# Performance work log

Measured on AMD Instinct MI355X. Metric: run time of the kernel, lower is better.

The kernel has to match this reference:

```python
import jax, jax.numpy as jnp
import numpy as np

B, M, D = 16384, 32, 16
LAYERS = [64, 64, 64]


def setup_inputs() -> dict:
    key = jax.random.key(0)
    ks = jax.random.split(key, 4)
    inp = {"embeddings": jax.random.normal(ks[0], (B, M, D), dtype=jnp.float32)}
    hk_1 = M
    for i, hk in enumerate(LAYERS):
        # glorot-ish scale for W_i of shape (m, Hk_1, Hk)
        scale = (2.0 / (M * hk_1 + hk)) ** 0.5
        inp[f"W{i}"] = jax.random.normal(ks[i + 1], (M, hk_1, hk), dtype=jnp.float32) * scale
        hk_1 = hk
    return inp


def reference(embeddings, W0, W1, W2):
    # embeddings == x0: (B, m, D); W_i: (m, Hk_1, Hk)
    x0 = embeddings
    xk = x0  # x^{k-1}, starts as x0 with Hk_1 = m
    outs = []
    for W in (W0, W1, W2):
        # Fused form of: (x0[:,:,None,:] * xk[:,None,:,:])[..., None] * W -> sum over m, Hk_1
        # then permute to (B, Hk, D) and apply activation.
        xk = jax.nn.relu(jnp.einsum("bmd,bhd,mhk->bkd", x0, xk, W))  # (B, Hk, D)
        outs.append(jnp.sum(xk, axis=2))  # (B, Hk)
    return jnp.concatenate(outs, axis=1)  # (B, sum(layers_dim))
```

## Files before the change

### kernel.cpp

```cpp
#include <hip/hip_runtime.h>


typedef _Float16 half8 __attribute__((ext_vector_type(8)));
typedef _Float16 half2v __attribute__((ext_vector_type(2)));
typedef float f32x4 __attribute__((ext_vector_type(4)));

#define OUT_STRIDE 192
#define X0R 32
#define X0B 512
#define XKR 72
#define XKB 1152

__global__ void prep_w_all(const float* __restrict__ W0,
                           const float* __restrict__ W1,
                           const float* __restrict__ W2,
                           _Float16* __restrict__ dst) {
  int e = blockIdx.x * 256 + threadIdx.x;
  const float* W;
  int logH, nkbLog, le;
  if (e < 65536)       { W = W0; logH = 5; nkbLog = 5; le = e; }
  else if (e < 196608) { W = W1; logH = 6; nkbLog = 6; le = e - 65536; }
  else                 { W = W2; logH = 6; nkbLog = 6; le = e - 196608; }
  int j    = le & 7;
  int lane = (le >> 3) & 63;
  int rr   = lane & 15, qq = lane >> 4;
  int rest = le >> 9;
  int kb   = rest & ((1 << nkbLog) - 1);
  int t    = rest >> nkbLog;
  int k    = kb * 32 + qq * 8 + j;
  int H    = 1 << logH;
  int m    = k >> logH, h = k & (H - 1);
  int n    = t * 16 + rr;
  dst[e] = (_Float16)W[(m * H + h) * 64 + n];
}

template<int NHI, bool LAST>
__device__ __forceinline__ void run_layer(
    const _Float16* __restrict__ Wp, const half8 (&av)[4][NHI],
    const _Float16* x0s, _Float16* xkw, float* __restrict__ out,
    long gb0, int loff, int lane, int r, int q)
{
  const int NKB = 32 * NHI;
  f32x4 acc[4][4];
#pragma unroll
  for (int b = 0; b < 4; ++b)
#pragma unroll
    for (int t = 0; t < 4; ++t) acc[b][t] = (f32x4){0.f, 0.f, 0.f, 0.f};

  const _Float16* Wl = Wp + lane * 8;

#pragma unroll 2
  for (int m = 0; m < 32; ++m) {
    half2v xs2[4];
#pragma unroll
    for (int b = 0; b < 4; ++b) {
      _Float16 x = x0s[b * X0B + r * X0R + m];
      xs2[b] = (half2v){x, x};
    }
#pragma unroll
    for (int hi = 0; hi < NHI; ++hi) {
      const int kb = m * NHI + hi;
      half8 Bf[4];
#pragma unroll
      for (int t = 0; t < 4; ++t)
        Bf[t] = *(const half8*)(Wl + (size_t)(t * NKB + kb) * 512);
#pragma unroll
      for (int b = 0; b < 4; ++b) {
        half8 af;
        half2v* ap = (half2v*)&af;
        const half2v* vp = (const half2v*)&av[b][hi];
#pragma unroll
        for (int j2 = 0; j2 < 4; ++j2) ap[j2] = vp[j2] * xs2[b];
#pragma unroll
        for (int t = 0; t < 4; ++t)
          acc[b][t] = __builtin_amdgcn_mfma_f32_16x16x32_f16(
              af, Bf[t], acc[b][t], 0, 0, 0);
      }
    }
  }

#pragma unroll
  for (int b = 0; b < 4; ++b) {
#pragma unroll
    for (int t = 0; t < 4; ++t) {
      float s = 0.f;
#pragma unroll
      for (int rr = 0; rr < 4; ++rr) {
        float v = acc[b][t][rr];
        v = v > 0.f ? v : 0.f;
        s += v;
        if (!LAST)
          xkw[b * XKB + (q * 4 + rr) * XKR + t * 16 + r] = (_Float16)v;
      }
      s += __shfl_xor(s, 16);
      s += __shfl_xor(s, 32);
      if (q == 0)
        out[(gb0 + b) * OUT_STRIDE + loff + t * 16 + r] = s;
    }
  }
}

__global__ __launch_bounds__(256, 3) void cin_main(
    const float* __restrict__ emb, const _Float16* __restrict__ Wall,
    float* __restrict__ out)
{
  __shared__ __align__(16) _Float16 lds[16 * X0B + 16 * XKB];
  const int lane = threadIdx.x & 63;
  const int wv = threadIdx.x >> 6;
  const int r = lane & 15, q = lane >> 4;
  const long gb0 = (long)blockIdx.x * 16 + wv * 4;

  _Float16* x0w = &lds[wv * 4 * X0B];
  _Float16* xkw = &lds[16 * X0B + wv * 4 * XKB];

#pragma unroll
  for (int bb = 0; bb < 4; ++bb) {
    const float* src = emb + (gb0 + bb) * 512;
    _Float16* dstb = x0w + bb * X0B;
#pragma unroll
    for (int i = 0; i < 2; ++i) {
      int f = i * 256 + lane * 4;
      float4 v = *(const float4*)(src + f);
      int m = f >> 4, d = f & 15;
      dstb[(d + 0) * X0R + m] = (_Float16)v.x;
      dstb[(d + 1) * X0R + m] = (_Float16)v.y;
      dstb[(d + 2) * X0R + m] = (_Float16)v.z;
      dstb[(d + 3) * X0R + m] = (_Float16)v.w;
    }
  }

  half8 av1[4][1];
#pragma unroll
  for (int b = 0; b < 4; ++b)
    av1[b][0] = *(const half8*)(x0w + b * X0B + r * X0R + q * 8);
  run_layer<1, false>(Wall, av1, x0w, xkw, out, gb0, 0, lane, r, q);

  half8 av2[4][2];
#pragma unroll
  for (int b = 0; b < 4; ++b)
#pragma unroll
    for (int hi = 0; hi < 2; ++hi)
      av2[b][hi] = *(const half8*)(xkw + b * XKB + r * XKR + hi * 32 + q * 8);
  run_layer<2, false>(Wall + 65536, av2, x0w, xkw, out, gb0, 64, lane, r, q);

#pragma unroll
  for (int b = 0; b < 4; ++b)
#pragma unroll
    for (int hi = 0; hi < 2; ++hi)
      av2[b][hi] = *(const half8*)(xkw + b * XKB + r * XKR + hi * 32 + q * 8);
  run_layer<2, true>(Wall + 196608, av2, x0w, xkw, out, gb0, 128, lane, r, q);
}

extern "C" void kernel_launch(void* const* d_in, const int* in_sizes, int n_in,
                              void* d_out, int out_size, void* d_ws, size_t ws_size,
                              hipStream_t stream) {
  const float* emb = (const float*)d_in[0];
  const float* W0  = (const float*)d_in[1];
  const float* W1  = (const float*)d_in[2];
  const float* W2  = (const float*)d_in[3];
  float* out = (float*)d_out;
  _Float16* ws = (_Float16*)d_ws;

  prep_w_all<<<1280, 256, 0, stream>>>(W0, W1, W2, ws);

  cin_main<<<1024, 256, 0, stream>>>(emb, ws, out);
}
```

Before: 206.4 us.

## Pad x0 LDS rows and reorder packed W by k-block with tiled prep

Pads the x0 shared-memory row stride from 32 to 33 halves to reduce LDS bank conflicts on the transposed stores and broadcast reads. The A-fragment load becomes eight scalar half loads, since the padded rows are no longer 16-byte aligned. The packed fp16 weight layout is reordered so that the four n-tiles of each k-block are contiguous, making the per-iteration B loads more local. The prep kernel now stages each 32x64 slab through padded shared memory with coalesced reads and vector writes, using 160 blocks instead of 1280.

```diff
diff --git a/kernel.cpp b/kernel.cpp
--- a/kernel.cpp
+++ b/kernel.cpp
@@ -6,8 +6,8 @@
 typedef float f32x4 __attribute__((ext_vector_type(4)));
 
 #define OUT_STRIDE 192
-#define X0R 32
-#define X0B 512
+#define X0R 33
+#define X0B (16 * X0R)
 #define XKR 72
 #define XKB 1152
 
@@ -15,55 +15,56 @@
                            const float* __restrict__ W1,
                            const float* __restrict__ W2,
                            _Float16* __restrict__ dst) {
-  int e = blockIdx.x * 256 + threadIdx.x;
-  const float* W;
-  int logH, nkbLog, le;
-  if (e < 65536)       { W = W0; logH = 5; nkbLog = 5; le = e; }
-  else if (e < 196608) { W = W1; logH = 6; nkbLog = 6; le = e - 65536; }
-  else                 { W = W2; logH = 6; nkbLog = 6; le = e - 196608; }
-  int j    = le & 7;
-  int lane = (le >> 3) & 63;
-  int rr   = lane & 15, qq = lane >> 4;
-  int rest = le >> 9;
-  int kb   = rest & ((1 << nkbLog) - 1);
-  int t    = rest >> nkbLog;
-  int k    = kb * 32 + qq * 8 + j;
-  int H    = 1 << logH;
-  int m    = k >> logH, h = k & (H - 1);
-  int n    = t * 16 + rr;
-  dst[e] = (_Float16)W[(m * H + h) * 64 + n];
+  __shared__ float tile[32 * 65];
+  const int tid = threadIdx.x;
+  const int blk = blockIdx.x;
+  const float* src;
+  _Float16* d;
+  int kb;
+  if (blk < 32)      { src = W0 + (size_t)blk * 2048;        d = dst;          kb = blk; }
+  else if (blk < 96) { src = W1 + (size_t)(blk - 32) * 2048; d = dst + 65536;  kb = blk - 32; }
+  else               { src = W2 + (size_t)(blk - 96) * 2048; d = dst + 196608; kb = blk - 96; }
+#pragma unroll
+  for (int i = tid; i < 2048; i += 256)
+    tile[(i >> 6) * 65 + (i & 63)] = src[i];
+  __syncthreads();
+  const int lane = tid & 63, t = tid >> 6;
+  const int qq = lane >> 4, n = t * 16 + (lane & 15);
+  half8 v;
+#pragma unroll
+  for (int j = 0; j < 8; ++j)
+    v[j] = (_Float16)tile[(qq * 8 + j) * 65 + n];
+  *(half8*)(d + (size_t)kb * 2048 + tid * 8) = v;
 }
 
 template<int NHI, bool LAST>
 __device__ __forceinline__ void run_layer(
     const _Float16* __restrict__ Wp, const half8 (&av)[4][NHI],
-    const _Float16* x0s, _Float16* xkw, float* __restrict__ out,
+    const _Float16* x0row0, _Float16* xkw, float* __restrict__ out,
     long gb0, int loff, int lane, int r, int q)
 {
-  const int NKB = 32 * NHI;
   f32x4 acc[4][4];
 #pragma unroll
   for (int b = 0; b < 4; ++b)
 #pragma unroll
     for (int t = 0; t < 4; ++t) acc[b][t] = (f32x4){0.f, 0.f, 0.f, 0.f};
 
-  const _Float16* Wl = Wp + lane * 8;
-
 #pragma unroll 2
   for (int m = 0; m < 32; ++m) {
     half2v xs2[4];
 #pragma unroll
     for (int b = 0; b < 4; ++b) {
-      _Float16 x = x0s[b * X0B + r * X0R + m];
+      _Float16 x = x0row0[b * X0B + m];
       xs2[b] = (half2v){x, x};
     }
 #pragma unroll
     for (int hi = 0; hi < NHI; ++hi) {
       const int kb = m * NHI + hi;
+      const _Float16* pkb = Wp + (size_t)kb * 2048 + lane * 8;
       half8 Bf[4];
 #pragma unroll
       for (int t = 0; t < 4; ++t)
-        Bf[t] = *(const half8*)(Wl + (size_t)(t * NKB + kb) * 512);
+        Bf[t] = *(const half8*)(pkb + t * 512);
 #pragma unroll
       for (int b = 0; b < 4; ++b) {
         half8 af;
@@ -129,11 +130,15 @@
     }
   }
 
+  const _Float16* x0row0 = x0w + r * X0R;
+
   half8 av1[4][1];
 #pragma unroll
   for (int b = 0; b < 4; ++b)
-    av1[b][0] = *(const half8*)(x0w + b * X0B + r * X0R + q * 8);
-  run_layer<1, false>(Wall, av1, x0w, xkw, out, gb0, 0, lane, r, q);
+#pragma unroll
+    for (int j = 0; j < 8; ++j)
+      av1[b][0][j] = x0row0[b * X0B + q * 8 + j];
+  run_layer<1, false>(Wall, av1, x0row0, xkw, out, gb0, 0, lane, r, q);
 
   half8 av2[4][2];
 #pragma unroll
@@ -141,14 +146,14 @@
 #pragma unroll
     for (int hi = 0; hi < 2; ++hi)
       av2[b][hi] = *(const half8*)(xkw + b * XKB + r * XKR + hi * 32 + q * 8);
-  run_layer<2, false>(Wall + 65536, av2, x0w, xkw, out, gb0, 64, lane, r, q);
+  run_layer<2, false>(Wall + 65536, av2, x0row0, xkw, out, gb0, 64, lane, r, q);
 
 #pragma unroll
   for (int b = 0; b < 4; ++b)
 #pragma unroll
     for (int hi = 0; hi < 2; ++hi)
       av2[b][hi] = *(const half8*)(xkw + b * XKB + r * XKR + hi * 32 + q * 8);
-  run_layer<2, true>(Wall + 196608, av2, x0w, xkw, out, gb0, 128, lane, r, q);
+  run_layer<2, true>(Wall + 196608, av2, x0row0, xkw, out, gb0, 128, lane, r, q);
 }
 
 extern "C" void kernel_launch(void* const* d_in, const int* in_sizes, int n_in,
@@ -161,7 +166,7 @@
   float* out = (float*)d_out;
   _Float16* ws = (_Float16*)d_ws;
 
-  prep_w_all<<<1280, 256, 0, stream>>>(W0, W1, W2, ws);
+  prep_w_all<<<160, 256, 0, stream>>>(W0, W1, W2, ws);
 
   cin_main<<<1024, 256, 0, stream>>>(emb, ws, out);
 }
```

After: 209.9 us. About the same (+1.7%).
